# Kernel optimization log

Hardware: AMD Instinct MI355X
Metric: run time of the kernel (lower is better)

The kernel has to match this reference:

```python
import jax, jax.numpy as jnp
import numpy as np

D_MODEL = 1024
N_HEAD = 16
HEAD_DIM = D_MODEL // N_HEAD
B, S = 4, 2048


def setup_inputs() -> dict:
    key = jax.random.key(0)
    ks = jax.random.split(key, 11)
    s = 1.0 / np.sqrt(D_MODEL)
    return {
        "query": jax.random.normal(ks[0], (B, S, D_MODEL), jnp.float32),
        "key": jax.random.normal(ks[1], (B, S, D_MODEL), jnp.float32),
        "value": jax.random.normal(ks[2], (B, S, D_MODEL), jnp.float32),
        "Wq": jax.random.normal(ks[3], (D_MODEL, D_MODEL), jnp.float32) * s,
        "bq": jax.random.normal(ks[4], (D_MODEL,), jnp.float32) * s,
        "Wk": jax.random.normal(ks[5], (D_MODEL, D_MODEL), jnp.float32) * s,
        "bk": jax.random.normal(ks[6], (D_MODEL,), jnp.float32) * s,
        "Wv": jax.random.normal(ks[7], (D_MODEL, D_MODEL), jnp.float32) * s,
        "bv": jax.random.normal(ks[8], (D_MODEL,), jnp.float32) * s,
        "Wo": jax.random.normal(ks[9], (D_MODEL, D_MODEL), jnp.float32) * s,
        "bo": jax.random.normal(ks[10], (D_MODEL,), jnp.float32) * s,
    }


def reference(query, key, value, Wq, bq, Wk, bk, Wv, bv, Wo, bo):
    b, s, d_model = query.shape
    # projections; reshape to [b, h, s, hd]
    def proj(x, W, bias):
        return (x @ W + bias).reshape(b, s, N_HEAD, HEAD_DIM).transpose(0, 2, 1, 3)
    q = proj(query, Wq, bq)
    k = proj(key, Wk, bk)
    v = proj(value, Wv, bv)
    # NOTE: original code scales by sqrt(d_model) (bug-faithful), not sqrt(head_dim)
    scores = jnp.einsum("bhqd,bhkd->bhqk", q, k) / jnp.sqrt(jnp.float32(d_model))
    causal = jnp.tril(jnp.ones((s, s), dtype=bool))
    scores = jnp.where(causal[None, None], scores, -jnp.inf)
    p = jax.nn.softmax(scores, axis=-1)  # dropout is identity in eval
    x = jnp.einsum("bhqk,bhkd->bhqd", p, v)
    x = x.transpose(0, 2, 1, 3).reshape(b, s, d_model)
    return x @ Wo + bo
```

## Files before the change

### kernel.cpp

```cpp
#include <hip/hip_runtime.h>
#include <hip/hip_bf16.h>
#include <cstdint>
#include <cstddef>

#define D_MODEL 1024
#define N_HEAD 16
#define HEAD_DIM 64
#define BATCH 4
#define SEQ 2048
#define M_ROWS (BATCH * SEQ)

typedef __attribute__((ext_vector_type(8))) short short8v;
typedef __attribute__((ext_vector_type(4))) float f32x4;
typedef __attribute__((ext_vector_type(16))) float f32x16;

__device__ __forceinline__ unsigned short f2bf(float f) {
    union { uint32_t i; float f; } c;
    c.f = f;
    uint32_t r = c.i + 0x7FFFu + ((c.i >> 16) & 1u);
    return (unsigned short)(r >> 16);
}
__device__ __forceinline__ unsigned short trunc_bf(float f) {
    return (unsigned short)(__float_as_uint(f) >> 16);
}
__device__ __forceinline__ uint32_t pack_trunc2(float a, float b) {
    return __builtin_amdgcn_perm(__float_as_uint(b), __float_as_uint(a), 0x07060302u);
}

struct __align__(16) U4 { uint32_t x, y, z, w; };
struct __align__(8) U2 { uint32_t x, y; };

__device__ __forceinline__ int sw_off(int row, int gl) {
    return row * 64 + ((gl ^ (row & 7)) << 3);
}

__device__ __forceinline__ void gload16(const unsigned short *g, unsigned short *l) {
    __builtin_amdgcn_global_load_lds((const __attribute__((address_space(1))) void *)g,
                                     (__attribute__((address_space(3))) void *)l, 16, 0, 0);
}

__global__ __launch_bounds__(256)
void cvt_kernel(const float *__restrict__ src, unsigned short *__restrict__ dst)
{
    const size_t i = ((size_t)blockIdx.x * 256 + threadIdx.x) * 8;
    float4 lo = *(const float4 *)(src + i);
    float4 hi = *(const float4 *)(src + i + 4);
    U4 pk;
    pk.x = pack_trunc2(lo.x, lo.y);
    pk.y = pack_trunc2(lo.z, lo.w);
    pk.z = pack_trunc2(hi.x, hi.y);
    pk.w = pack_trunc2(hi.z, hi.w);
    *(U4 *)(dst + i) = pk;
}

__global__ __launch_bounds__(256)
void wtrans_kernel(const float *__restrict__ W, unsigned short *__restrict__ Wt)
{
    __shared__ float tile[32][33];
    const int t = threadIdx.x;
    const int tx = t & 31, ty = t >> 5;
    const int bk = blockIdx.y * 32, bn = blockIdx.x * 32;
#pragma unroll
    for (int i = 0; i < 4; i++)
        tile[ty + 8 * i][tx] = W[(size_t)(bk + ty + 8 * i) * D_MODEL + bn + tx];
    __syncthreads();
#pragma unroll
    for (int i = 0; i < 4; i++)
        Wt[(size_t)(bn + ty + 8 * i) * D_MODEL + bk + tx] = trunc_bf(tile[tx][ty + 8 * i]);
}

template <typename TA, int MODE, typename TO>
__global__ __launch_bounds__(256, 2)
void mgemm_kernel(const TA *__restrict__ A,
                  const unsigned short *__restrict__ Wt,
                  const float *__restrict__ bias,
                  TO *__restrict__ out,
                  float escale)
{
    __shared__ __align__(16) unsigned short At[128 * 64];
    __shared__ __align__(16) unsigned short Bt[128 * 64];

    const int t = threadIdx.x;
    const int wave = t >> 6;
    const int lane = t & 63;
    const int n_ = lane & 15;
    const int quad = lane >> 4;
    const int wm = wave >> 1, wn = wave & 1;
    const int m0 = blockIdx.x * 128;
    const int n0 = blockIdx.y * 128;

    f32x4 acc[4][4];
#pragma unroll
    for (int i = 0; i < 4; i++)
#pragma unroll
        for (int j = 0; j < 4; j++) acc[i][j] = (f32x4){0.f, 0.f, 0.f, 0.f};

    const int srow = t >> 3;
    const int sg = t & 7;
    const int rl = lane >> 3;
    const int gsw = (lane & 7) ^ rl;

    for (int k0 = 0; k0 < D_MODEL; k0 += 64) {
        __syncthreads();
        if constexpr (sizeof(TA) == 2) {
#pragma unroll
            for (int c = 0; c < 4; c++) {
                const int rb = wave * 32 + c * 8;
                gload16((const unsigned short *)A + (size_t)(m0 + rb + rl) * D_MODEL + k0 + (gsw << 3),
                        &At[rb * 64]);
                gload16(Wt + (size_t)(n0 + rb + rl) * D_MODEL + k0 + (gsw << 3),
                        &Bt[rb * 64]);
            }
        } else {
#pragma unroll
            for (int i = 0; i < 4; i++) {
                const int r = srow + 32 * i;
                const float *p = (const float *)A + (size_t)(m0 + r) * D_MODEL + k0 + sg * 8;
                float4 lo = *(const float4 *)p;
                float4 hi = *(const float4 *)(p + 4);
                U4 pk;
                pk.x = pack_trunc2(lo.x, lo.y);
                pk.y = pack_trunc2(lo.z, lo.w);
                pk.z = pack_trunc2(hi.x, hi.y);
                pk.w = pack_trunc2(hi.z, hi.w);
                *(U4 *)&At[sw_off(r, sg)] = pk;
            }
#pragma unroll
            for (int i = 0; i < 4; i++) {
                const int r = srow + 32 * i;
                const unsigned short *p = Wt + (size_t)(n0 + r) * D_MODEL + k0 + sg * 8;
                *(U4 *)&Bt[sw_off(r, sg)] = *(const U4 *)p;
            }
        }
        __syncthreads();

#pragma unroll
        for (int c = 0; c < 2; c++) {
            short8v af[4], bf[4];
#pragma unroll
            for (int mt = 0; mt < 4; mt++)
                af[mt] = *(const short8v *)&At[sw_off(wm * 64 + mt * 16 + n_, c * 4 + quad)];
#pragma unroll
            for (int nt = 0; nt < 4; nt++)
                bf[nt] = *(const short8v *)&Bt[sw_off(wn * 64 + nt * 16 + n_, c * 4 + quad)];
#pragma unroll
            for (int mt = 0; mt < 4; mt++)
#pragma unroll
                for (int nt = 0; nt < 4; nt++)
                    acc[mt][nt] =
                        __builtin_amdgcn_mfma_f32_16x16x32_bf16(af[mt], bf[nt], acc[mt][nt], 0, 0, 0);
        }
    }

    float bi[4];
#pragma unroll
    for (int nt = 0; nt < 4; nt++) bi[nt] = bias[n0 + wn * 64 + nt * 16 + n_];

#pragma unroll
    for (int mt = 0; mt < 4; mt++) {
#pragma unroll
        for (int reg = 0; reg < 4; reg++) {
            const int m = m0 + wm * 64 + mt * 16 + quad * 4 + reg;
#pragma unroll
            for (int nt = 0; nt < 4; nt++) {
                const int col = n0 + wn * 64 + nt * 16 + n_;
                const float v = (acc[mt][nt][reg] + bi[nt]) * escale;
                if constexpr (MODE == 1) {
                    ((unsigned short *)out)[(size_t)m * D_MODEL + col] = f2bf(v);
                } else if constexpr (MODE == 2) {
                    const size_t idx = ((size_t)(m >> 11) * D_MODEL + col) * SEQ + (m & 2047);
                    ((unsigned short *)out)[idx] = f2bf(v);
                } else {
                    ((float *)out)[(size_t)m * D_MODEL + col] = v;
                }
            }
        }
    }
}

__global__ __launch_bounds__(256, 2)
void attn_kernel(const unsigned short *Qg,
                 const unsigned short *__restrict__ Kg,
                 const unsigned short *__restrict__ VTg,
                 unsigned short *AO)
{
    __shared__ __align__(16) unsigned short Kt[64 * 64];
    __shared__ __align__(16) unsigned short Vt[64 * 64];

    const int h = blockIdx.x;
    const int b = blockIdx.y;
    const int qpair = blockIdx.z;
    const int t = threadIdx.x;
    const int w = t >> 6;
    const int lane = t & 63;
    const int ql = lane & 31;
    const int hi = lane >> 5;

    const size_t row_base = (size_t)b * SEQ * D_MODEL + h * HEAD_DIM;
    const size_t vhead = (size_t)(b * N_HEAD + h) * HEAD_DIM * SEQ;

    const int r0 = t >> 3;
    const int g = t & 7;

#pragma unroll
    for (int pass = 0; pass < 2; ++pass) {
        const int qb = pass ? (15 - qpair) : qpair;
        const int qs0 = qb * 128 + w * 32;
        const int qseq = qs0 + ql;

        short8v qf[4];
#pragma unroll
        for (int c = 0; c < 4; c++)
            qf[c] = *(const short8v *)(Qg + row_base + (size_t)qseq * D_MODEL + c * 16 + hi * 8);

        float m_i = -INFINITY, l_i = 0.f;
        f32x16 Oacc[2];
#pragma unroll
        for (int dt = 0; dt < 2; dt++)
#pragma unroll
            for (int i = 0; i < 16; i++) Oacc[dt][i] = 0.f;

        const int kb_max = 2 * qb + 1;

        for (int kb = 0; kb <= kb_max; ++kb) {
            __syncthreads();
#pragma unroll
            for (int i = 0; i < 2; i++) {
                const int r = r0 + 32 * i;
                U4 kv = *(const U4 *)(Kg + row_base + (size_t)(kb * 64 + r) * D_MODEL + g * 8);
                *(U4 *)&Kt[sw_off(r, g)] = kv;
                U4 vv = *(const U4 *)(VTg + vhead + (size_t)r * SEQ + kb * 64 + g * 8);
                *(U4 *)&Vt[sw_off(r, g)] = vv;
            }
            __syncthreads();

            if (kb * 64 > qs0 + 31) continue;

            f32x16 st[2];
            __builtin_amdgcn_s_setprio(1);
#pragma unroll
            for (int kt = 0; kt < 2; kt++) {
#pragma unroll
                for (int i = 0; i < 16; i++) st[kt][i] = 0.f;
#pragma unroll
                for (int c = 0; c < 4; c++) {
                    short8v kf = *(const short8v *)&Kt[sw_off(kt * 32 + ql, c * 2 + hi)];
                    st[kt] = __builtin_amdgcn_mfma_f32_32x32x16_bf16(kf, qf[c], st[kt], 0, 0, 0);
                }
            }
            __builtin_amdgcn_s_setprio(0);

            if (kb * 64 + 63 > qs0) {
#pragma unroll
                for (int kt = 0; kt < 2; kt++)
#pragma unroll
                    for (int r = 0; r < 16; r++) {
                        const int kseq = kb * 64 + kt * 32 + (r & 3) + 8 * (r >> 2) + 4 * hi;
                        if (kseq > qseq) st[kt][r] = -INFINITY;
                    }
            }

            float mx = -INFINITY;
#pragma unroll
            for (int kt = 0; kt < 2; kt++)
#pragma unroll
                for (int r = 0; r < 16; r++) mx = fmaxf(mx, st[kt][r]);
            mx = fmaxf(mx, __shfl_xor(mx, 32, 64));
            const float mnew = fmaxf(m_i, mx);
            const float alpha = __builtin_amdgcn_exp2f(m_i - mnew);
            m_i = mnew;
            float rs = 0.f;
#pragma unroll
            for (int kt = 0; kt < 2; kt++)
#pragma unroll
                for (int r = 0; r < 16; r++) {
                    const float p = __builtin_amdgcn_exp2f(st[kt][r] - mnew);
                    st[kt][r] = p;
                    rs += p;
                }
            rs += __shfl_xor(rs, 32, 64);
            l_i = l_i * alpha + rs;
#pragma unroll
            for (int dt = 0; dt < 2; dt++)
#pragma unroll
                for (int r = 0; r < 16; r++) Oacc[dt][r] *= alpha;

            short8v pf[4];
#pragma unroll
            for (int tt = 0; tt < 4; tt++) {
                const int kt = tt >> 1, o = (tt & 1) * 8;
                const uint32_t A  = pack_trunc2(st[kt][o + 0], st[kt][o + 1]);
                const uint32_t A2 = pack_trunc2(st[kt][o + 2], st[kt][o + 3]);
                const uint32_t B  = pack_trunc2(st[kt][o + 4], st[kt][o + 5]);
                const uint32_t B2 = pack_trunc2(st[kt][o + 6], st[kt][o + 7]);
                const uint32_t c1 = (uint32_t)__shfl_xor((int)(hi ? A : B), 32, 64);
                const uint32_t c2 = (uint32_t)__shfl_xor((int)(hi ? A2 : B2), 32, 64);
                union { uint32_t u[4]; short8v s; } cv;
                cv.u[0] = hi ? c1 : A;
                cv.u[1] = hi ? c2 : A2;
                cv.u[2] = hi ? B : c1;
                cv.u[3] = hi ? B2 : c2;
                pf[tt] = cv.s;
            }

            __builtin_amdgcn_s_setprio(1);
#pragma unroll
            for (int dt = 0; dt < 2; dt++)
#pragma unroll
                for (int tt = 0; tt < 4; tt++) {
                    short8v vf = *(const short8v *)&Vt[sw_off(dt * 32 + ql, tt * 2 + hi)];
                    Oacc[dt] = __builtin_amdgcn_mfma_f32_32x32x16_bf16(vf, pf[tt], Oacc[dt], 0, 0, 0);
                }
            __builtin_amdgcn_s_setprio(0);
        }

        const float linv = 1.f / l_i;
        const size_t obase = row_base + (size_t)qseq * D_MODEL;
#pragma unroll
        for (int dt = 0; dt < 2; dt++)
#pragma unroll
            for (int rg = 0; rg < 4; rg++) {
                const int d0 = dt * 32 + 8 * rg + 4 * hi;
                U2 pk;
                pk.x = (uint32_t)f2bf(Oacc[dt][4 * rg + 0] * linv) |
                       ((uint32_t)f2bf(Oacc[dt][4 * rg + 1] * linv) << 16);
                pk.y = (uint32_t)f2bf(Oacc[dt][4 * rg + 2] * linv) |
                       ((uint32_t)f2bf(Oacc[dt][4 * rg + 3] * linv) << 16);
                *(U2 *)(AO + obase + d0) = pk;
            }
    }
}

extern "C" void kernel_launch(void *const *d_in, const int *in_sizes, int n_in,
                              void *d_out, int out_size, void *d_ws, size_t ws_size,
                              hipStream_t stream)
{
    const float *q  = (const float *)d_in[0];
    const float *k  = (const float *)d_in[1];
    const float *v  = (const float *)d_in[2];
    const float *Wq = (const float *)d_in[3];
    const float *bq = (const float *)d_in[4];
    const float *Wk = (const float *)d_in[5];
    const float *bk = (const float *)d_in[6];
    const float *Wv = (const float *)d_in[7];
    const float *bv = (const float *)d_in[8];
    const float *Wo = (const float *)d_in[9];
    const float *bo = (const float *)d_in[10];
    float *out = (float *)d_out;

    const size_t TENS = (size_t)M_ROWS * D_MODEL;
    unsigned short *qbuf = (unsigned short *)d_ws;
    unsigned short *kbuf = qbuf + TENS;
    unsigned short *vtbuf = kbuf + TENS;
    unsigned short *cbuf = vtbuf + TENS;
    unsigned short *wt_new = cbuf + TENS;
    unsigned short *wt_old = vtbuf + TENS;

    dim3 wgrid(32, 32);
    dim3 ggrid(M_ROWS / 128, D_MODEL / 128);
    const int cgrid = (int)(TENS / 8 / 256);

    const float qscale = 0.03125f * 1.44269504088896341f;

    const size_t need_new = (5 * TENS + (size_t)D_MODEL * D_MODEL) * sizeof(unsigned short);

    if (ws_size >= need_new) {
        unsigned short *wt = wt_new;
        wtrans_kernel<<<wgrid, 256, 0, stream>>>(Wq, wt);
        cvt_kernel<<<cgrid, 256, 0, stream>>>(q, cbuf);
        mgemm_kernel<unsigned short, 1, unsigned short><<<ggrid, 256, 0, stream>>>(cbuf, wt, bq, qbuf, qscale);
        wtrans_kernel<<<wgrid, 256, 0, stream>>>(Wk, wt);
        cvt_kernel<<<cgrid, 256, 0, stream>>>(k, cbuf);
        mgemm_kernel<unsigned short, 1, unsigned short><<<ggrid, 256, 0, stream>>>(cbuf, wt, bk, kbuf, 1.f);
        wtrans_kernel<<<wgrid, 256, 0, stream>>>(Wv, wt);
        cvt_kernel<<<cgrid, 256, 0, stream>>>(v, cbuf);
        mgemm_kernel<unsigned short, 2, unsigned short><<<ggrid, 256, 0, stream>>>(cbuf, wt, bv, vtbuf, 1.f);

        attn_kernel<<<dim3(N_HEAD, BATCH, SEQ / 256), 256, 0, stream>>>(qbuf, kbuf, vtbuf, qbuf);

        wtrans_kernel<<<wgrid, 256, 0, stream>>>(Wo, wt);
        mgemm_kernel<unsigned short, 3, float><<<ggrid, 256, 0, stream>>>(qbuf, wt, bo, out, 1.f);
    } else {
        unsigned short *wt = wt_old;
        wtrans_kernel<<<wgrid, 256, 0, stream>>>(Wq, wt);
        mgemm_kernel<float, 1, unsigned short><<<ggrid, 256, 0, stream>>>(q, wt, bq, qbuf, qscale);
        wtrans_kernel<<<wgrid, 256, 0, stream>>>(Wk, wt);
        mgemm_kernel<float, 1, unsigned short><<<ggrid, 256, 0, stream>>>(k, wt, bk, kbuf, 1.f);
        wtrans_kernel<<<wgrid, 256, 0, stream>>>(Wv, wt);
        mgemm_kernel<float, 2, unsigned short><<<ggrid, 256, 0, stream>>>(v, wt, bv, vtbuf, 1.f);

        attn_kernel<<<dim3(N_HEAD, BATCH, SEQ / 256), 256, 0, stream>>>(qbuf, kbuf, vtbuf, qbuf);

        wtrans_kernel<<<wgrid, 256, 0, stream>>>(Wo, wt);
        mgemm_kernel<unsigned short, 3, float><<<ggrid, 256, 0, stream>>>(qbuf, wt, bo, out, 1.f);
    }
}
```

Baseline: 323.0 us.

## Batch Q/K/V weight transposes, conversions and projections into single grouped launches

```diff
diff --git a/kernel.cpp b/kernel.cpp
--- a/kernel.cpp
+++ b/kernel.cpp
@@ -26,6 +26,9 @@
 __device__ __forceinline__ uint32_t pack_trunc2(float a, float b) {
     return __builtin_amdgcn_perm(__float_as_uint(b), __float_as_uint(a), 0x07060302u);
 }
+__device__ __forceinline__ uint32_t pack_rne2(float a, float b) {
+    return (uint32_t)f2bf(a) | ((uint32_t)f2bf(b) << 16);
+}
 
 struct __align__(16) U4 { uint32_t x, y, z, w; };
 struct __align__(8) U2 { uint32_t x, y; };
@@ -40,8 +43,14 @@
 }
 
 __global__ __launch_bounds__(256)
-void cvt_kernel(const float *__restrict__ src, unsigned short *__restrict__ dst)
-{
+void cvt3_kernel(const float *__restrict__ q, const float *__restrict__ k,
+                 const float *__restrict__ v,
+                 unsigned short *__restrict__ cq, unsigned short *__restrict__ ck,
+                 unsigned short *__restrict__ cv)
+{
+    const int z = blockIdx.y;
+    const float *src = z == 0 ? q : (z == 1 ? k : v);
+    unsigned short *dst = z == 0 ? cq : (z == 1 ? ck : cv);
     const size_t i = ((size_t)blockIdx.x * 256 + threadIdx.x) * 8;
     float4 lo = *(const float4 *)(src + i);
     float4 hi = *(const float4 *)(src + i + 4);
@@ -53,8 +62,8 @@
     *(U4 *)(dst + i) = pk;
 }
 
-__global__ __launch_bounds__(256)
-void wtrans_kernel(const float *__restrict__ W, unsigned short *__restrict__ Wt)
+__device__ __forceinline__ void wtrans_body(const float *__restrict__ W,
+                                            unsigned short *__restrict__ Wt)
 {
     __shared__ float tile[32][33];
     const int t = threadIdx.x;
@@ -69,16 +78,39 @@
         Wt[(size_t)(bn + ty + 8 * i) * D_MODEL + bk + tx] = trunc_bf(tile[tx][ty + 8 * i]);
 }
 
-template <typename TA, int MODE, typename TO>
-__global__ __launch_bounds__(256, 2)
-void mgemm_kernel(const TA *__restrict__ A,
-                  const unsigned short *__restrict__ Wt,
-                  const float *__restrict__ bias,
-                  TO *__restrict__ out,
-                  float escale)
+__global__ __launch_bounds__(256)
+void wtrans_kernel(const float *__restrict__ W, unsigned short *__restrict__ Wt)
+{
+    wtrans_body(W, Wt);
+}
+
+__global__ __launch_bounds__(256)
+void wtrans3_kernel(const float *__restrict__ W0, const float *__restrict__ W1,
+                    const float *__restrict__ W2, unsigned short *__restrict__ Wt3)
+{
+    const int z = blockIdx.z;
+    wtrans_body(z == 0 ? W0 : (z == 1 ? W1 : W2),
+                Wt3 + (size_t)z * D_MODEL * D_MODEL);
+}
+
+__global__ __launch_bounds__(256, 3)
+void qkv_gemm_kernel(const unsigned short *__restrict__ cq,
+                     const unsigned short *__restrict__ ck,
+                     const unsigned short *__restrict__ cv,
+                     const unsigned short *__restrict__ Wt3,
+                     const float *__restrict__ bq, const float *__restrict__ bk,
+                     const float *__restrict__ bv,
+                     unsigned short *__restrict__ oq, unsigned short *__restrict__ ok,
+                     unsigned short *__restrict__ ov,
+                     float qscale)
 {
     __shared__ __align__(16) unsigned short At[128 * 64];
     __shared__ __align__(16) unsigned short Bt[128 * 64];
+
+    const int z = blockIdx.z;
+    const unsigned short *A = z == 0 ? cq : (z == 1 ? ck : cv);
+    const unsigned short *Wt = Wt3 + (size_t)z * D_MODEL * D_MODEL;
+    const float *bias = z == 0 ? bq : (z == 1 ? bk : bv);
 
     const int t = threadIdx.x;
     const int wave = t >> 6;
@@ -95,6 +127,98 @@
 #pragma unroll
         for (int j = 0; j < 4; j++) acc[i][j] = (f32x4){0.f, 0.f, 0.f, 0.f};
 
+    const int rl = lane >> 3;
+    const int gsw = (lane & 7) ^ rl;
+
+    for (int k0 = 0; k0 < D_MODEL; k0 += 64) {
+        __syncthreads();
+#pragma unroll
+        for (int c = 0; c < 4; c++) {
+            const int rb = wave * 32 + c * 8;
+            gload16(A + (size_t)(m0 + rb + rl) * D_MODEL + k0 + (gsw << 3), &At[rb * 64]);
+            gload16(Wt + (size_t)(n0 + rb + rl) * D_MODEL + k0 + (gsw << 3), &Bt[rb * 64]);
+        }
+        __syncthreads();
+
+#pragma unroll
+        for (int c = 0; c < 2; c++) {
+            short8v af[4], bf[4];
+#pragma unroll
+            for (int mt = 0; mt < 4; mt++)
+                af[mt] = *(const short8v *)&At[sw_off(wm * 64 + mt * 16 + n_, c * 4 + quad)];
+#pragma unroll
+            for (int nt = 0; nt < 4; nt++)
+                bf[nt] = *(const short8v *)&Bt[sw_off(wn * 64 + nt * 16 + n_, c * 4 + quad)];
+#pragma unroll
+            for (int mt = 0; mt < 4; mt++)
+#pragma unroll
+                for (int nt = 0; nt < 4; nt++)
+                    acc[mt][nt] =
+                        __builtin_amdgcn_mfma_f32_16x16x32_bf16(af[mt], bf[nt], acc[mt][nt], 0, 0, 0);
+        }
+    }
+
+    float bi[4];
+#pragma unroll
+    for (int nt = 0; nt < 4; nt++) bi[nt] = bias[n0 + wn * 64 + nt * 16 + n_];
+
+    if (z < 2) {
+        unsigned short *out = z == 0 ? oq : ok;
+        const float es = z == 0 ? qscale : 1.f;
+#pragma unroll
+        for (int mt = 0; mt < 4; mt++)
+#pragma unroll
+            for (int reg = 0; reg < 4; reg++) {
+                const int m = m0 + wm * 64 + mt * 16 + quad * 4 + reg;
+#pragma unroll
+                for (int nt = 0; nt < 4; nt++) {
+                    const int col = n0 + wn * 64 + nt * 16 + n_;
+                    out[(size_t)m * D_MODEL + col] = f2bf((acc[mt][nt][reg] + bi[nt]) * es);
+                }
+            }
+    } else {
+#pragma unroll
+        for (int mt = 0; mt < 4; mt++) {
+            const int m = m0 + wm * 64 + mt * 16 + quad * 4;
+#pragma unroll
+            for (int nt = 0; nt < 4; nt++) {
+                const int col = n0 + wn * 64 + nt * 16 + n_;
+                const size_t idx = ((size_t)(m >> 11) * D_MODEL + col) * SEQ + (m & 2047);
+                U2 pk;
+                pk.x = pack_rne2(acc[mt][nt][0] + bi[nt], acc[mt][nt][1] + bi[nt]);
+                pk.y = pack_rne2(acc[mt][nt][2] + bi[nt], acc[mt][nt][3] + bi[nt]);
+                *(U2 *)(ov + idx) = pk;
+            }
+        }
+    }
+}
+
+template <typename TA, int MODE, typename TO>
+__global__ __launch_bounds__(256, 3)
+void mgemm_kernel(const TA *__restrict__ A,
+                  const unsigned short *__restrict__ Wt,
+                  const float *__restrict__ bias,
+                  TO *__restrict__ out,
+                  float escale)
+{
+    __shared__ __align__(16) unsigned short At[128 * 64];
+    __shared__ __align__(16) unsigned short Bt[128 * 64];
+
+    const int t = threadIdx.x;
+    const int wave = t >> 6;
+    const int lane = t & 63;
+    const int n_ = lane & 15;
+    const int quad = lane >> 4;
+    const int wm = wave >> 1, wn = wave & 1;
+    const int m0 = blockIdx.x * 128;
+    const int n0 = blockIdx.y * 128;
+
+    f32x4 acc[4][4];
+#pragma unroll
+    for (int i = 0; i < 4; i++)
+#pragma unroll
+        for (int j = 0; j < 4; j++) acc[i][j] = (f32x4){0.f, 0.f, 0.f, 0.f};
+
     const int srow = t >> 3;
     const int sg = t & 7;
     const int rl = lane >> 3;
@@ -108,8 +232,7 @@
                 const int rb = wave * 32 + c * 8;
                 gload16((const unsigned short *)A + (size_t)(m0 + rb + rl) * D_MODEL + k0 + (gsw << 3),
                         &At[rb * 64]);
-                gload16(Wt + (size_t)(n0 + rb + rl) * D_MODEL + k0 + (gsw << 3),
-                        &Bt[rb * 64]);
+                gload16(Wt + (size_t)(n0 + rb + rl) * D_MODEL + k0 + (gsw << 3), &Bt[rb * 64]);
             }
         } else {
 #pragma unroll
@@ -156,25 +279,36 @@
 #pragma unroll
     for (int nt = 0; nt < 4; nt++) bi[nt] = bias[n0 + wn * 64 + nt * 16 + n_];
 
-#pragma unroll
-    for (int mt = 0; mt < 4; mt++) {
-#pragma unroll
-        for (int reg = 0; reg < 4; reg++) {
-            const int m = m0 + wm * 64 + mt * 16 + quad * 4 + reg;
+    if constexpr (MODE == 2) {
+#pragma unroll
+        for (int mt = 0; mt < 4; mt++) {
+            const int m = m0 + wm * 64 + mt * 16 + quad * 4;
 #pragma unroll
             for (int nt = 0; nt < 4; nt++) {
                 const int col = n0 + wn * 64 + nt * 16 + n_;
-                const float v = (acc[mt][nt][reg] + bi[nt]) * escale;
-                if constexpr (MODE == 1) {
-                    ((unsigned short *)out)[(size_t)m * D_MODEL + col] = f2bf(v);
-                } else if constexpr (MODE == 2) {
-                    const size_t idx = ((size_t)(m >> 11) * D_MODEL + col) * SEQ + (m & 2047);
-                    ((unsigned short *)out)[idx] = f2bf(v);
-                } else {
-                    ((float *)out)[(size_t)m * D_MODEL + col] = v;
+                const size_t idx = ((size_t)(m >> 11) * D_MODEL + col) * SEQ + (m & 2047);
+                U2 pk;
+                pk.x = pack_rne2(acc[mt][nt][0] + bi[nt], acc[mt][nt][1] + bi[nt]);
+                pk.y = pack_rne2(acc[mt][nt][2] + bi[nt], acc[mt][nt][3] + bi[nt]);
+                *(U2 *)((unsigned short *)out + idx) = pk;
+            }
+        }
+    } else {
+#pragma unroll
+        for (int mt = 0; mt < 4; mt++)
+#pragma unroll
+            for (int reg = 0; reg < 4; reg++) {
+                const int m = m0 + wm * 64 + mt * 16 + quad * 4 + reg;
+#pragma unroll
+                for (int nt = 0; nt < 4; nt++) {
+                    const int col = n0 + wn * 64 + nt * 16 + n_;
+                    const float v = (acc[mt][nt][reg] + bi[nt]) * escale;
+                    if constexpr (MODE == 1)
+                        ((unsigned short *)out)[(size_t)m * D_MODEL + col] = f2bf(v);
+                    else
+                        ((float *)out)[(size_t)m * D_MODEL + col] = v;
                 }
             }
-        }
     }
 }
 
@@ -349,39 +483,38 @@
     float *out = (float *)d_out;
 
     const size_t TENS = (size_t)M_ROWS * D_MODEL;
-    unsigned short *qbuf = (unsigned short *)d_ws;
-    unsigned short *kbuf = qbuf + TENS;
-    unsigned short *vtbuf = kbuf + TENS;
-    unsigned short *cbuf = vtbuf + TENS;
-    unsigned short *wt_new = cbuf + TENS;
-    unsigned short *wt_old = vtbuf + TENS;
+    const size_t WT = (size_t)D_MODEL * D_MODEL;
 
     dim3 wgrid(32, 32);
     dim3 ggrid(M_ROWS / 128, D_MODEL / 128);
-    const int cgrid = (int)(TENS / 8 / 256);
-
     const float qscale = 0.03125f * 1.44269504088896341f;
 
-    const size_t need_new = (5 * TENS + (size_t)D_MODEL * D_MODEL) * sizeof(unsigned short);
-
-    if (ws_size >= need_new) {
-        unsigned short *wt = wt_new;
-        wtrans_kernel<<<wgrid, 256, 0, stream>>>(Wq, wt);
-        cvt_kernel<<<cgrid, 256, 0, stream>>>(q, cbuf);
-        mgemm_kernel<unsigned short, 1, unsigned short><<<ggrid, 256, 0, stream>>>(cbuf, wt, bq, qbuf, qscale);
-        wtrans_kernel<<<wgrid, 256, 0, stream>>>(Wk, wt);
-        cvt_kernel<<<cgrid, 256, 0, stream>>>(k, cbuf);
-        mgemm_kernel<unsigned short, 1, unsigned short><<<ggrid, 256, 0, stream>>>(cbuf, wt, bk, kbuf, 1.f);
-        wtrans_kernel<<<wgrid, 256, 0, stream>>>(Wv, wt);
-        cvt_kernel<<<cgrid, 256, 0, stream>>>(v, cbuf);
-        mgemm_kernel<unsigned short, 2, unsigned short><<<ggrid, 256, 0, stream>>>(cbuf, wt, bv, vtbuf, 1.f);
+    const size_t need_fused = (4 * TENS + 3 * WT) * sizeof(unsigned short);
+
+    if (ws_size >= need_fused && (size_t)out_size >= 2 * TENS * sizeof(unsigned short)) {
+        unsigned short *cq = (unsigned short *)d_out;
+        unsigned short *ck = cq + TENS;
+        unsigned short *cv_ = (unsigned short *)d_ws;
+        unsigned short *qbuf = cv_ + TENS;
+        unsigned short *kbuf = qbuf + TENS;
+        unsigned short *vtbuf = kbuf + TENS;
+        unsigned short *wt3 = vtbuf + TENS;
+
+        wtrans3_kernel<<<dim3(32, 32, 3), 256, 0, stream>>>(Wq, Wk, Wv, wt3);
+        cvt3_kernel<<<dim3((int)(TENS / 8 / 256), 3), 256, 0, stream>>>(q, k, v, cq, ck, cv_);
+        qkv_gemm_kernel<<<dim3(M_ROWS / 128, D_MODEL / 128, 3), 256, 0, stream>>>(
+            cq, ck, cv_, wt3, bq, bk, bv, qbuf, kbuf, vtbuf, qscale);
 
         attn_kernel<<<dim3(N_HEAD, BATCH, SEQ / 256), 256, 0, stream>>>(qbuf, kbuf, vtbuf, qbuf);
 
-        wtrans_kernel<<<wgrid, 256, 0, stream>>>(Wo, wt);
-        mgemm_kernel<unsigned short, 3, float><<<ggrid, 256, 0, stream>>>(qbuf, wt, bo, out, 1.f);
+        wtrans_kernel<<<wgrid, 256, 0, stream>>>(Wo, wt3);
+        mgemm_kernel<unsigned short, 3, float><<<ggrid, 256, 0, stream>>>(qbuf, wt3, bo, out, 1.f);
     } else {
-        unsigned short *wt = wt_old;
+        unsigned short *qbuf = (unsigned short *)d_ws;
+        unsigned short *kbuf = qbuf + TENS;
+        unsigned short *vtbuf = kbuf + TENS;
+        unsigned short *wt = vtbuf + TENS;
+
         wtrans_kernel<<<wgrid, 256, 0, stream>>>(Wq, wt);
         mgemm_kernel<float, 1, unsigned short><<<ggrid, 256, 0, stream>>>(q, wt, bq, qbuf, qscale);
         wtrans_kernel<<<wgrid, 256, 0, stream>>>(Wk, wt);
```

Measured after the change: 376.2 us. +16.5%, slower.

## Double-buffer LDS tiles in bf16 GEMM and vectorize transposed V stores

Applied to the files above, without the earlier changes.

```diff
diff --git a/kernel.cpp b/kernel.cpp
--- a/kernel.cpp
+++ b/kernel.cpp
@@ -25,6 +25,9 @@
 }
 __device__ __forceinline__ uint32_t pack_trunc2(float a, float b) {
     return __builtin_amdgcn_perm(__float_as_uint(b), __float_as_uint(a), 0x07060302u);
+}
+__device__ __forceinline__ uint32_t pack_rne2(float a, float b) {
+    return (uint32_t)f2bf(a) | ((uint32_t)f2bf(b) << 16);
 }
 
 struct __align__(16) U4 { uint32_t x, y, z, w; };
@@ -77,8 +80,8 @@
                   TO *__restrict__ out,
                   float escale)
 {
-    __shared__ __align__(16) unsigned short At[128 * 64];
-    __shared__ __align__(16) unsigned short Bt[128 * 64];
+    __shared__ __align__(16) unsigned short At[2][128 * 64];
+    __shared__ __align__(16) unsigned short Bt[2][128 * 64];
 
     const int t = threadIdx.x;
     const int wave = t >> 6;
@@ -100,18 +103,57 @@
     const int rl = lane >> 3;
     const int gsw = (lane & 7) ^ rl;
 
-    for (int k0 = 0; k0 < D_MODEL; k0 += 64) {
-        __syncthreads();
-        if constexpr (sizeof(TA) == 2) {
-#pragma unroll
-            for (int c = 0; c < 4; c++) {
-                const int rb = wave * 32 + c * 8;
-                gload16((const unsigned short *)A + (size_t)(m0 + rb + rl) * D_MODEL + k0 + (gsw << 3),
-                        &At[rb * 64]);
-                gload16(Wt + (size_t)(n0 + rb + rl) * D_MODEL + k0 + (gsw << 3),
-                        &Bt[rb * 64]);
-            }
-        } else {
+    if constexpr (sizeof(TA) == 2) {
+        const unsigned short *Ab = (const unsigned short *)A;
+#pragma unroll
+        for (int c = 0; c < 4; c++) {
+            const int rb = wave * 32 + c * 8;
+            gload16(Ab + (size_t)(m0 + rb + rl) * D_MODEL + (gsw << 3), &At[0][rb * 64]);
+            gload16(Wt + (size_t)(n0 + rb + rl) * D_MODEL + (gsw << 3), &Bt[0][rb * 64]);
+        }
+#pragma unroll 2
+        for (int kt = 0; kt < 16; ++kt) {
+            const int cur = kt & 1;
+            if (kt < 15) {
+                const int k1 = (kt + 1) * 64;
+#pragma unroll
+                for (int c = 0; c < 4; c++) {
+                    const int rb = wave * 32 + c * 8;
+                    gload16(Ab + (size_t)(m0 + rb + rl) * D_MODEL + k1 + (gsw << 3),
+                            &At[cur ^ 1][rb * 64]);
+                    gload16(Wt + (size_t)(n0 + rb + rl) * D_MODEL + k1 + (gsw << 3),
+                            &Bt[cur ^ 1][rb * 64]);
+                }
+                asm volatile("s_waitcnt vmcnt(8)" ::: "memory");
+            } else {
+                asm volatile("s_waitcnt vmcnt(0)" ::: "memory");
+            }
+            __builtin_amdgcn_sched_barrier(0);
+            __builtin_amdgcn_s_barrier();
+            __builtin_amdgcn_sched_barrier(0);
+
+#pragma unroll
+            for (int c = 0; c < 2; c++) {
+                short8v af[4], bf[4];
+#pragma unroll
+                for (int mt = 0; mt < 4; mt++)
+                    af[mt] = *(const short8v *)&At[cur][sw_off(wm * 64 + mt * 16 + n_, c * 4 + quad)];
+#pragma unroll
+                for (int nt = 0; nt < 4; nt++)
+                    bf[nt] = *(const short8v *)&Bt[cur][sw_off(wn * 64 + nt * 16 + n_, c * 4 + quad)];
+#pragma unroll
+                for (int mt = 0; mt < 4; mt++)
+#pragma unroll
+                    for (int nt = 0; nt < 4; nt++)
+                        acc[mt][nt] = __builtin_amdgcn_mfma_f32_16x16x32_bf16(
+                            af[mt], bf[nt], acc[mt][nt], 0, 0, 0);
+            }
+            __builtin_amdgcn_sched_barrier(0);
+            __builtin_amdgcn_s_barrier();
+        }
+    } else {
+        for (int k0 = 0; k0 < D_MODEL; k0 += 64) {
+            __syncthreads();
 #pragma unroll
             for (int i = 0; i < 4; i++) {
                 const int r = srow + 32 * i;
@@ -123,32 +165,31 @@
                 pk.y = pack_trunc2(lo.z, lo.w);
                 pk.z = pack_trunc2(hi.x, hi.y);
                 pk.w = pack_trunc2(hi.z, hi.w);
-                *(U4 *)&At[sw_off(r, sg)] = pk;
+                *(U4 *)&At[0][sw_off(r, sg)] = pk;
             }
 #pragma unroll
             for (int i = 0; i < 4; i++) {
                 const int r = srow + 32 * i;
                 const unsigned short *p = Wt + (size_t)(n0 + r) * D_MODEL + k0 + sg * 8;
-                *(U4 *)&Bt[sw_off(r, sg)] = *(const U4 *)p;
-            }
-        }
-        __syncthreads();
-
-#pragma unroll
-        for (int c = 0; c < 2; c++) {
-            short8v af[4], bf[4];
-#pragma unroll
-            for (int mt = 0; mt < 4; mt++)
-                af[mt] = *(const short8v *)&At[sw_off(wm * 64 + mt * 16 + n_, c * 4 + quad)];
-#pragma unroll
-            for (int nt = 0; nt < 4; nt++)
-                bf[nt] = *(const short8v *)&Bt[sw_off(wn * 64 + nt * 16 + n_, c * 4 + quad)];
-#pragma unroll
-            for (int mt = 0; mt < 4; mt++)
+                *(U4 *)&Bt[0][sw_off(r, sg)] = *(const U4 *)p;
+            }
+            __syncthreads();
+#pragma unroll
+            for (int c = 0; c < 2; c++) {
+                short8v af[4], bf[4];
+#pragma unroll
+                for (int mt = 0; mt < 4; mt++)
+                    af[mt] = *(const short8v *)&At[0][sw_off(wm * 64 + mt * 16 + n_, c * 4 + quad)];
 #pragma unroll
                 for (int nt = 0; nt < 4; nt++)
-                    acc[mt][nt] =
-                        __builtin_amdgcn_mfma_f32_16x16x32_bf16(af[mt], bf[nt], acc[mt][nt], 0, 0, 0);
+                    bf[nt] = *(const short8v *)&Bt[0][sw_off(wn * 64 + nt * 16 + n_, c * 4 + quad)];
+#pragma unroll
+                for (int mt = 0; mt < 4; mt++)
+#pragma unroll
+                    for (int nt = 0; nt < 4; nt++)
+                        acc[mt][nt] = __builtin_amdgcn_mfma_f32_16x16x32_bf16(
+                            af[mt], bf[nt], acc[mt][nt], 0, 0, 0);
+            }
         }
     }
 
@@ -156,25 +197,36 @@
 #pragma unroll
     for (int nt = 0; nt < 4; nt++) bi[nt] = bias[n0 + wn * 64 + nt * 16 + n_];
 
-#pragma unroll
-    for (int mt = 0; mt < 4; mt++) {
-#pragma unroll
-        for (int reg = 0; reg < 4; reg++) {
-            const int m = m0 + wm * 64 + mt * 16 + quad * 4 + reg;
+    if constexpr (MODE == 2) {
+#pragma unroll
+        for (int mt = 0; mt < 4; mt++) {
+            const int m = m0 + wm * 64 + mt * 16 + quad * 4;
 #pragma unroll
             for (int nt = 0; nt < 4; nt++) {
                 const int col = n0 + wn * 64 + nt * 16 + n_;
-                const float v = (acc[mt][nt][reg] + bi[nt]) * escale;
-                if constexpr (MODE == 1) {
-                    ((unsigned short *)out)[(size_t)m * D_MODEL + col] = f2bf(v);
-                } else if constexpr (MODE == 2) {
-                    const size_t idx = ((size_t)(m >> 11) * D_MODEL + col) * SEQ + (m & 2047);
-                    ((unsigned short *)out)[idx] = f2bf(v);
-                } else {
-                    ((float *)out)[(size_t)m * D_MODEL + col] = v;
+                const size_t idx = ((size_t)(m >> 11) * D_MODEL + col) * SEQ + (m & 2047);
+                U2 pk;
+                pk.x = pack_rne2(acc[mt][nt][0] + bi[nt], acc[mt][nt][1] + bi[nt]);
+                pk.y = pack_rne2(acc[mt][nt][2] + bi[nt], acc[mt][nt][3] + bi[nt]);
+                *(U2 *)((unsigned short *)out + idx) = pk;
+            }
+        }
+    } else {
+#pragma unroll
+        for (int mt = 0; mt < 4; mt++)
+#pragma unroll
+            for (int reg = 0; reg < 4; reg++) {
+                const int m = m0 + wm * 64 + mt * 16 + quad * 4 + reg;
+#pragma unroll
+                for (int nt = 0; nt < 4; nt++) {
+                    const int col = n0 + wn * 64 + nt * 16 + n_;
+                    const float v = (acc[mt][nt][reg] + bi[nt]) * escale;
+                    if constexpr (MODE == 1)
+                        ((unsigned short *)out)[(size_t)m * D_MODEL + col] = f2bf(v);
+                    else
+                        ((float *)out)[(size_t)m * D_MODEL + col] = v;
                 }
             }
-        }
     }
 }
 
@@ -349,6 +401,8 @@
     float *out = (float *)d_out;
 
     const size_t TENS = (size_t)M_ROWS * D_MODEL;
+    const size_t WT = (size_t)D_MODEL * D_MODEL;
+
     unsigned short *qbuf = (unsigned short *)d_ws;
     unsigned short *kbuf = qbuf + TENS;
     unsigned short *vtbuf = kbuf + TENS;
@@ -362,7 +416,7 @@
 
     const float qscale = 0.03125f * 1.44269504088896341f;
 
-    const size_t need_new = (5 * TENS + (size_t)D_MODEL * D_MODEL) * sizeof(unsigned short);
+    const size_t need_new = (5 * TENS + WT) * sizeof(unsigned short);
 
     if (ws_size >= need_new) {
         unsigned short *wt = wt_new;
```

Measured after the change: 323.4 us. About the same (+0.1%).

## Shrink GEMM M-tile to 64, vectorize V-transpose stores, add lazy softmax rescale

Applied to the files above, without the earlier changes.

```diff
diff --git a/kernel.cpp b/kernel.cpp
--- a/kernel.cpp
+++ b/kernel.cpp
@@ -25,6 +25,9 @@
 }
 __device__ __forceinline__ uint32_t pack_trunc2(float a, float b) {
     return __builtin_amdgcn_perm(__float_as_uint(b), __float_as_uint(a), 0x07060302u);
+}
+__device__ __forceinline__ uint32_t pack_rne2(float a, float b) {
+    return (uint32_t)f2bf(a) | ((uint32_t)f2bf(b) << 16);
 }
 
 struct __align__(16) U4 { uint32_t x, y, z, w; };
@@ -70,14 +73,14 @@
 }
 
 template <typename TA, int MODE, typename TO>
-__global__ __launch_bounds__(256, 2)
+__global__ __launch_bounds__(256, 4)
 void mgemm_kernel(const TA *__restrict__ A,
                   const unsigned short *__restrict__ Wt,
                   const float *__restrict__ bias,
                   TO *__restrict__ out,
                   float escale)
 {
-    __shared__ __align__(16) unsigned short At[128 * 64];
+    __shared__ __align__(16) unsigned short At[64 * 64];
     __shared__ __align__(16) unsigned short Bt[128 * 64];
 
     const int t = threadIdx.x;
@@ -86,12 +89,12 @@
     const int n_ = lane & 15;
     const int quad = lane >> 4;
     const int wm = wave >> 1, wn = wave & 1;
-    const int m0 = blockIdx.x * 128;
+    const int m0 = blockIdx.x * 64;
     const int n0 = blockIdx.y * 128;
 
-    f32x4 acc[4][4];
-#pragma unroll
-    for (int i = 0; i < 4; i++)
+    f32x4 acc[2][4];
+#pragma unroll
+    for (int i = 0; i < 2; i++)
 #pragma unroll
         for (int j = 0; j < 4; j++) acc[i][j] = (f32x4){0.f, 0.f, 0.f, 0.f};
 
@@ -103,17 +106,20 @@
     for (int k0 = 0; k0 < D_MODEL; k0 += 64) {
         __syncthreads();
         if constexpr (sizeof(TA) == 2) {
+            const unsigned short *Ab = (const unsigned short *)A;
+#pragma unroll
+            for (int c = 0; c < 2; c++) {
+                const int rb = wave * 8 + c * 32;
+                gload16(Ab + (size_t)(m0 + rb + rl) * D_MODEL + k0 + (gsw << 3), &At[rb * 64]);
+            }
 #pragma unroll
             for (int c = 0; c < 4; c++) {
-                const int rb = wave * 32 + c * 8;
-                gload16((const unsigned short *)A + (size_t)(m0 + rb + rl) * D_MODEL + k0 + (gsw << 3),
-                        &At[rb * 64]);
-                gload16(Wt + (size_t)(n0 + rb + rl) * D_MODEL + k0 + (gsw << 3),
-                        &Bt[rb * 64]);
+                const int rb = wave * 8 + c * 32;
+                gload16(Wt + (size_t)(n0 + rb + rl) * D_MODEL + k0 + (gsw << 3), &Bt[rb * 64]);
             }
         } else {
 #pragma unroll
-            for (int i = 0; i < 4; i++) {
+            for (int i = 0; i < 2; i++) {
                 const int r = srow + 32 * i;
                 const float *p = (const float *)A + (size_t)(m0 + r) * D_MODEL + k0 + sg * 8;
                 float4 lo = *(const float4 *)p;
@@ -136,19 +142,19 @@
 
 #pragma unroll
         for (int c = 0; c < 2; c++) {
-            short8v af[4], bf[4];
-#pragma unroll
-            for (int mt = 0; mt < 4; mt++)
-                af[mt] = *(const short8v *)&At[sw_off(wm * 64 + mt * 16 + n_, c * 4 + quad)];
+            short8v af[2], bf[4];
+#pragma unroll
+            for (int mt = 0; mt < 2; mt++)
+                af[mt] = *(const short8v *)&At[sw_off(wm * 32 + mt * 16 + n_, c * 4 + quad)];
 #pragma unroll
             for (int nt = 0; nt < 4; nt++)
                 bf[nt] = *(const short8v *)&Bt[sw_off(wn * 64 + nt * 16 + n_, c * 4 + quad)];
 #pragma unroll
-            for (int mt = 0; mt < 4; mt++)
+            for (int mt = 0; mt < 2; mt++)
 #pragma unroll
                 for (int nt = 0; nt < 4; nt++)
-                    acc[mt][nt] =
-                        __builtin_amdgcn_mfma_f32_16x16x32_bf16(af[mt], bf[nt], acc[mt][nt], 0, 0, 0);
+                    acc[mt][nt] = __builtin_amdgcn_mfma_f32_16x16x32_bf16(
+                        af[mt], bf[nt], acc[mt][nt], 0, 0, 0);
         }
     }
 
@@ -156,25 +162,36 @@
 #pragma unroll
     for (int nt = 0; nt < 4; nt++) bi[nt] = bias[n0 + wn * 64 + nt * 16 + n_];
 
-#pragma unroll
-    for (int mt = 0; mt < 4; mt++) {
-#pragma unroll
-        for (int reg = 0; reg < 4; reg++) {
-            const int m = m0 + wm * 64 + mt * 16 + quad * 4 + reg;
+    if constexpr (MODE == 2) {
+#pragma unroll
+        for (int mt = 0; mt < 2; mt++) {
+            const int m = m0 + wm * 32 + mt * 16 + quad * 4;
 #pragma unroll
             for (int nt = 0; nt < 4; nt++) {
                 const int col = n0 + wn * 64 + nt * 16 + n_;
-                const float v = (acc[mt][nt][reg] + bi[nt]) * escale;
-                if constexpr (MODE == 1) {
-                    ((unsigned short *)out)[(size_t)m * D_MODEL + col] = f2bf(v);
-                } else if constexpr (MODE == 2) {
-                    const size_t idx = ((size_t)(m >> 11) * D_MODEL + col) * SEQ + (m & 2047);
-                    ((unsigned short *)out)[idx] = f2bf(v);
-                } else {
-                    ((float *)out)[(size_t)m * D_MODEL + col] = v;
+                const size_t idx = ((size_t)(m >> 11) * D_MODEL + col) * SEQ + (m & 2047);
+                U2 pk;
+                pk.x = pack_rne2(acc[mt][nt][0] + bi[nt], acc[mt][nt][1] + bi[nt]);
+                pk.y = pack_rne2(acc[mt][nt][2] + bi[nt], acc[mt][nt][3] + bi[nt]);
+                *(U2 *)((unsigned short *)out + idx) = pk;
+            }
+        }
+    } else {
+#pragma unroll
+        for (int mt = 0; mt < 2; mt++)
+#pragma unroll
+            for (int reg = 0; reg < 4; reg++) {
+                const int m = m0 + wm * 32 + mt * 16 + quad * 4 + reg;
+#pragma unroll
+                for (int nt = 0; nt < 4; nt++) {
+                    const int col = n0 + wn * 64 + nt * 16 + n_;
+                    const float v = (acc[mt][nt][reg] + bi[nt]) * escale;
+                    if constexpr (MODE == 1)
+                        ((unsigned short *)out)[(size_t)m * D_MODEL + col] = f2bf(v);
+                    else
+                        ((float *)out)[(size_t)m * D_MODEL + col] = v;
                 }
             }
-        }
     }
 }
 
@@ -266,24 +283,39 @@
 #pragma unroll
                 for (int r = 0; r < 16; r++) mx = fmaxf(mx, st[kt][r]);
             mx = fmaxf(mx, __shfl_xor(mx, 32, 64));
-            const float mnew = fmaxf(m_i, mx);
-            const float alpha = __builtin_amdgcn_exp2f(m_i - mnew);
-            m_i = mnew;
-            float rs = 0.f;
-#pragma unroll
-            for (int kt = 0; kt < 2; kt++)
-#pragma unroll
-                for (int r = 0; r < 16; r++) {
-                    const float p = __builtin_amdgcn_exp2f(st[kt][r] - mnew);
-                    st[kt][r] = p;
-                    rs += p;
-                }
-            rs += __shfl_xor(rs, 32, 64);
-            l_i = l_i * alpha + rs;
-#pragma unroll
-            for (int dt = 0; dt < 2; dt++)
-#pragma unroll
-                for (int r = 0; r < 16; r++) Oacc[dt][r] *= alpha;
+
+            if (__all(mx <= m_i + 8.f)) {
+                float rs = 0.f;
+#pragma unroll
+                for (int kt = 0; kt < 2; kt++)
+#pragma unroll
+                    for (int r = 0; r < 16; r++) {
+                        const float p = __builtin_amdgcn_exp2f(st[kt][r] - m_i);
+                        st[kt][r] = p;
+                        rs += p;
+                    }
+                rs += __shfl_xor(rs, 32, 64);
+                l_i += rs;
+            } else {
+                const float mnew = fmaxf(m_i, mx);
+                const float alpha = __builtin_amdgcn_exp2f(m_i - mnew);
+                m_i = mnew;
+                float rs = 0.f;
+#pragma unroll
+                for (int kt = 0; kt < 2; kt++)
+#pragma unroll
+                    for (int r = 0; r < 16; r++) {
+                        const float p = __builtin_amdgcn_exp2f(st[kt][r] - mnew);
+                        st[kt][r] = p;
+                        rs += p;
+                    }
+                rs += __shfl_xor(rs, 32, 64);
+                l_i = l_i * alpha + rs;
+#pragma unroll
+                for (int dt = 0; dt < 2; dt++)
+#pragma unroll
+                    for (int r = 0; r < 16; r++) Oacc[dt][r] *= alpha;
+            }
 
             short8v pf[4];
 #pragma unroll
@@ -349,6 +381,8 @@
     float *out = (float *)d_out;
 
     const size_t TENS = (size_t)M_ROWS * D_MODEL;
+    const size_t WT = (size_t)D_MODEL * D_MODEL;
+
     unsigned short *qbuf = (unsigned short *)d_ws;
     unsigned short *kbuf = qbuf + TENS;
     unsigned short *vtbuf = kbuf + TENS;
@@ -357,12 +391,12 @@
     unsigned short *wt_old = vtbuf + TENS;
 
     dim3 wgrid(32, 32);
-    dim3 ggrid(M_ROWS / 128, D_MODEL / 128);
+    dim3 ggrid(M_ROWS / 64, D_MODEL / 128);
     const int cgrid = (int)(TENS / 8 / 256);
 
     const float qscale = 0.03125f * 1.44269504088896341f;
 
-    const size_t need_new = (5 * TENS + (size_t)D_MODEL * D_MODEL) * sizeof(unsigned short);
+    const size_t need_new = (5 * TENS + WT) * sizeof(unsigned short);
 
     if (ws_size >= need_new) {
         unsigned short *wt = wt_new;
```

Result: slower. 334.7 us (+3.6%).
